# Kernel optimization log

Hardware: AMD Instinct MI355X
Metric: run time of the kernel (lower is better)

Reference implementation:

```python
import jax, jax.numpy as jnp
import numpy as np
import math

DEPTH = 3
RATIO = 0.5
EPS = 1e-5


def _mlp_ln(h, W1, b1, W2, b2, W3, b3, g, beta):
    h = jax.nn.gelu(h @ W1 + b1, approximate=False)
    h = jax.nn.gelu(h @ W2 + b2, approximate=False)
    h = h @ W3 + b3
    mu = jnp.mean(h, axis=-1, keepdims=True)
    var = jnp.mean((h - mu) ** 2, axis=-1, keepdims=True)
    return g * (h - mu) * jax.lax.rsqrt(var + EPS) + beta


def _node_to_node(x, s, r, n, p):
    # two-way gather -> scatter_add -> MLP+LN. Row n of x_pad is a zero dummy
    # node that absorbs edges dropped by pooling (fixed-size, jit-friendly).
    x_pad = jnp.concatenate([x, jnp.zeros((1, x.shape[1]), x.dtype)], axis=0)
    msg = x_pad[jnp.concatenate([s, r])]            # [2E, C]
    recv = jnp.concatenate([r, s])                  # [2E]
    agg = jax.ops.segment_sum(msg, recv, num_segments=n + 1)[:n]
    return _mlp_ln(agg, *p)


def _forward(x, senders, receivers, pool_w, down_p, up_p):
    s, r = senders, receivers
    xs, edges, perms = [x], [(s, r)], []
    n = x.shape[0]
    for i in range(DEPTH):
        k = math.ceil(RATIO * n)  # PyG topk: ceil(ratio * N)
        w = pool_w[i]
        score = jnp.tanh(x @ w / jnp.linalg.norm(w))
        vals, perm = jax.lax.top_k(score, k)
        x = x[perm] * vals[:, None]
        # remap edges; dropped nodes (and old dummy n) map to new dummy k
        nmap = jnp.full((n + 1,), k, dtype=s.dtype).at[perm].set(
            jnp.arange(k, dtype=s.dtype))
        ns_, nr_ = nmap[s], nmap[r]
        invalid = (ns_ == k) | (nr_ == k)
        s = jnp.where(invalid, k, ns_)
        r = jnp.where(invalid, k, nr_)
        x = _node_to_node(x, s, r, k, down_p[i])
        if i < DEPTH - 1:
            xs.append(x)
            edges.append((s, r))
        perms.append(perm)
        n = k
    for i in range(DEPTH):
        j = DEPTH - 1 - i
        res = xs[j]
        s, r = edges[j]
        perm = perms[j]
        up = jnp.zeros_like(res).at[perm].set(x)
        x = jnp.concatenate([res, up], axis=-1)  # sum_res=False -> concat
        x = _node_to_node(x, s, r, res.shape[0], up_p[i])
    return x


def setup_inputs() -> dict:
    key = jax.random.key(0)
    ks = jax.random.split(key, 16)
    N, E, C, D = 50000, 600000, 128, DEPTH
    f32 = jnp.float32

    def lin(k, fi, fo):
        return (jax.random.normal(k, (D, fi, fo), f32) / np.sqrt(fi)).astype(f32)

    return {
        'x': jax.random.normal(ks[0], (N, C), f32),
        'senders': jax.random.randint(ks[1], (E,), 0, N, dtype=jnp.int32),
        'receivers': jax.random.randint(ks[2], (E,), 0, N, dtype=jnp.int32),
        'pool_w': jax.random.normal(ks[3], (D, C), f32),
        'down_W1': lin(ks[4], C, C), 'down_b1': jnp.zeros((D, C), f32),
        'down_W2': lin(ks[5], C, C), 'down_b2': jnp.zeros((D, C), f32),
        'down_W3': lin(ks[6], C, C), 'down_b3': jnp.zeros((D, C), f32),
        'down_g': jnp.ones((D, C), f32), 'down_beta': jnp.zeros((D, C), f32),
        'up_W1': lin(ks[7], 2 * C, C), 'up_b1': jnp.zeros((D, C), f32),
        'up_W2': lin(ks[8], C, C), 'up_b2': jnp.zeros((D, C), f32),
        'up_W3': lin(ks[9], C, C), 'up_b3': jnp.zeros((D, C), f32),
        'up_g': jnp.ones((D, C), f32), 'up_beta': jnp.zeros((D, C), f32),
    }


def reference(x, senders, receivers, pool_w,
              down_W1, down_b1, down_W2, down_b2, down_W3, down_b3,
              down_g, down_beta,
              up_W1, up_b1, up_W2, up_b2, up_W3, up_b3, up_g, up_beta):
    down_p = [(down_W1[i], down_b1[i], down_W2[i], down_b2[i],
               down_W3[i], down_b3[i], down_g[i], down_beta[i])
              for i in range(DEPTH)]
    up_p = [(up_W1[i], up_b1[i], up_W2[i], up_b2[i],
             up_W3[i], up_b3[i], up_g[i], up_beta[i])
            for i in range(DEPTH)]
    return _forward(x, senders, receivers, pool_w, down_p, up_p)
```

## Files before the change

### kernel.cpp

```cpp
#include <hip/hip_runtime.h>
#include <math.h>


typedef unsigned short u16;
typedef short bf16x8 __attribute__((ext_vector_type(8)));
typedef float f32x4 __attribute__((ext_vector_type(4)));

#define HIST_STRIDE (2 * 65536 + 512)
#define NB 128
#define NB_LOG 7
#define SUBR 5000

__device__ __forceinline__ unsigned int fkey(float f) {
  unsigned int b = __float_as_uint(f);
  return (b & 0x80000000u) ? ~b : (b | 0x80000000u);
}

__device__ __forceinline__ float gelu_f(float v) {
  return 0.5f * v * (1.0f + erff(v * 0.70710678118654752f));
}

__device__ __forceinline__ u16 f2bf(float f) {
  unsigned u = __float_as_uint(f);
  u = (u + 0x7FFFu + ((u >> 16) & 1u)) >> 16;
  return (u16)u;
}
__device__ __forceinline__ float bf2f(u16 u) {
  return __uint_as_float(((unsigned)u) << 16);
}

__global__ void score_kernel(const float* __restrict__ x, const float* __restrict__ w,
                             float* __restrict__ key, float* __restrict__ valt, int n) {
  int wave = threadIdx.x >> 6, lane = threadIdx.x & 63;
  int i = blockIdx.x * 4 + wave;
  if (i >= n) return;
  float2 xv = *(const float2*)&x[(size_t)i * 128 + lane * 2];
  float2 wv = *(const float2*)&w[lane * 2];
  double d  = (double)xv.x * wv.x + (double)xv.y * wv.y;
  double nw = (double)wv.x * wv.x + (double)wv.y * wv.y;
  for (int o = 32; o; o >>= 1) { d += __shfl_down(d, o, 64); nw += __shfl_down(nw, o, 64); }
  if (lane == 0) {
    key[i]  = (float)d;
    valt[i] = (float)tanh(d / sqrt(nw));
  }
}

__global__ void preamble_kernel(const float* __restrict__ x, u16* __restrict__ xb, int n,
                                const float* __restrict__ uW1, const float* __restrict__ uW2,
                                const float* __restrict__ uW3, u16* __restrict__ wt1,
                                u16* __restrict__ wt2, u16* __restrict__ wt3,
                                const float* __restrict__ poolw, double* __restrict__ sqn,
                                u16* __restrict__ z0, u16* __restrict__ z1,
                                u16* __restrict__ z2, int* __restrict__ histAll,
                                int nbX, int nbHZ, int nHist) {
  int b = blockIdx.x;
  if (b < nbX) {
    int gid = b * 256 + threadIdx.x;
    if (gid < n * 32) {
      float4 a = *(const float4*)&x[(size_t)gid * 4];
      *(ushort4*)&xb[(size_t)gid * 4] =
          make_ushort4(f2bf(a.x), f2bf(a.y), f2bf(a.z), f2bf(a.w));
    }
    return;
  }
  b -= nbX;
  if (b < 768) {
    int i = b * 256 + threadIdx.x;
    int lvl = i >> 16, rem = i & 65535;
    if (rem < 32768) {
      int k = rem >> 7, c = rem & 127;
      wt1[(size_t)lvl * 32768 + c * 256 + k] = f2bf(uW1[(size_t)lvl * 32768 + rem]);
    } else if (rem < 49152) {
      int j = rem - 32768; int k = j >> 7, c = j & 127;
      wt2[(size_t)lvl * 16384 + c * 128 + k] = f2bf(uW2[(size_t)lvl * 16384 + j]);
    } else {
      int j = rem - 49152; int k = j >> 7, c = j & 127;
      wt3[(size_t)lvl * 16384 + c * 128 + k] = f2bf(uW3[(size_t)lvl * 16384 + j]);
    }
    return;
  }
  b -= 768;
  if (b == 0) {
    if (threadIdx.x < 64) {
      int lane = threadIdx.x;
      for (int l = 0; l < 3; ++l) {
        float2 wv = *(const float2*)&poolw[l * 128 + lane * 2];
        double nw = (double)wv.x * wv.x + (double)wv.y * wv.y;
        for (int o = 32; o; o >>= 1) nw += __shfl_down(nw, o, 64);
        if (lane == 0) sqn[l] = sqrt(nw);
      }
    }
    return;
  }
  b -= 1;
  if (b == 0) {
    int t = threadIdx.x;
    if (t < 128) { z0[t] = 0; z1[t] = 0; z2[t] = 0; }
    return;
  }
  b -= 1;
  {
    int i = b * 256 + threadIdx.x;
    if (i < nHist) histAll[i] = 0;
  }
}

__global__ void hist_hi_kernel(const float* __restrict__ key, int* __restrict__ hist,
                               int* __restrict__ csum, int n) {
  __shared__ int lc[256];
  lc[threadIdx.x] = 0;
  __syncthreads();
  int i = blockIdx.x * 256 + threadIdx.x;
  if (i < n) {
    unsigned b = fkey(key[i]) >> 16;
    atomicAdd(&hist[b], 1);
    atomicAdd(&lc[b >> 8], 1);
  }
  __syncthreads();
  int v = lc[threadIdx.x];
  if (v) atomicAdd(&csum[threadIdx.x], v);
}

__global__ void hist_lo_kernel(const float* __restrict__ key, const int* __restrict__ meta,
                               int* __restrict__ hist, int* __restrict__ csum, int n) {
  __shared__ int lc[256];
  lc[threadIdx.x] = 0;
  __syncthreads();
  int i = blockIdx.x * 256 + threadIdx.x;
  if (i < n) {
    unsigned u = fkey(key[i]);
    if ((u >> 16) == (unsigned)meta[0]) {
      unsigned b = u & 0xFFFFu;
      atomicAdd(&hist[b], 1);
      atomicAdd(&lc[b >> 8], 1);
    }
  }
  __syncthreads();
  int v = lc[threadIdx.x];
  if (v) atomicAdd(&csum[threadIdx.x], v);
}

__device__ __forceinline__ void suffix_scan256(int* sA, int t) {
  for (int o = 1; o < 256; o <<= 1) {
    int add = (t + o < 256) ? sA[t + o] : 0;
    __syncthreads();
    sA[t] += add;
    __syncthreads();
  }
}

__global__ void find_hi2_kernel(const int* __restrict__ hist, const int* __restrict__ csum,
                                int* __restrict__ meta, int k) {
  __shared__ int sA[256];
  __shared__ int cSh, cumSh;
  int t = threadIdx.x;
  sA[t] = csum[t];
  __syncthreads();
  suffix_scan256(sA, t);
  int nxt = (t == 255) ? 0 : sA[t + 1];
  if (sA[t] >= k && nxt < k) { cSh = t; cumSh = nxt; }
  __syncthreads();
  int c = cSh;
  int k2 = k - cumSh;
  sA[t] = hist[c * 256 + t];
  __syncthreads();
  suffix_scan256(sA, t);
  nxt = (t == 255) ? 0 : sA[t + 1];
  if (sA[t] >= k2 && nxt < k2) {
    meta[0] = c * 256 + t;
    meta[1] = k2 - nxt;
  }
}

__global__ void find_lo2_kernel(const int* __restrict__ hist, const int* __restrict__ csum,
                                int* __restrict__ meta) {
  __shared__ int sA[256];
  __shared__ int cSh, cumSh;
  int t = threadIdx.x;
  int m = meta[1], B = meta[0];
  sA[t] = csum[t];
  __syncthreads();
  suffix_scan256(sA, t);
  int nxt = (t == 255) ? 0 : sA[t + 1];
  if (sA[t] >= m && nxt < m) { cSh = t; cumSh = nxt; }
  __syncthreads();
  int c = cSh;
  int m2 = m - cumSh;
  sA[t] = hist[c * 256 + t];
  __syncthreads();
  suffix_scan256(sA, t);
  nxt = (t == 255) ? 0 : sA[t + 1];
  if (sA[t] >= m2 && nxt < m2) {
    meta[3] = (int)((((unsigned)B) << 16) | (unsigned)(c * 256 + t));
    meta[4] = m2 - nxt;
  }
  if (t == 0) meta[5] = 0;
}

__global__ void tie_count_kernel(const float* __restrict__ key, const int* __restrict__ meta,
                                 int* __restrict__ tcnt, int n) {
  __shared__ int cnt[4];
  unsigned uT = (unsigned)meta[3];
  int i = blockIdx.x * 256 + threadIdx.x;
  bool tie = (i < n) && (fkey(key[i]) == uT);
  unsigned long long m = __ballot(tie);
  int lane = threadIdx.x & 63, w = threadIdx.x >> 6;
  if (lane == 0) cnt[w] = __popcll(m);
  __syncthreads();
  if (threadIdx.x == 0) tcnt[blockIdx.x] = cnt[0] + cnt[1] + cnt[2] + cnt[3];
}

__global__ void tie_select_kernel(const float* __restrict__ key, const float* __restrict__ valt,
                                  const int* __restrict__ tcnt, int* __restrict__ meta,
                                  int* __restrict__ perm, float* __restrict__ vals,
                                  int* __restrict__ nmap, int n, int k) {
  __shared__ int red[256];
  __shared__ int woff[4];
  int t = threadIdx.x;
  red[t] = (t < (int)blockIdx.x) ? tcnt[t] : 0;
  __syncthreads();
  for (int s = 128; s; s >>= 1) {
    if (t < s) red[t] += red[t + s];
    __syncthreads();
  }
  int blockbase = red[0];
  unsigned uT = (unsigned)meta[3];
  int tsel = meta[4];
  int i = blockIdx.x * 256 + t;
  unsigned u = (i < n) ? fkey(key[i]) : 0u;
  bool tie = (i < n) && (u == uT);
  unsigned long long m = __ballot(tie);
  int lane = t & 63, w = t >> 6;
  if (lane == 0) woff[w] = __popcll(m);
  __syncthreads();
  if (t == 0) {
    int c = 0;
    for (int q = 0; q < 4; ++q) { int v = woff[q]; woff[q] = c; c += v; }
  }
  __syncthreads();
  if (i > n) return;
  if (i == n) { nmap[n] = k; return; }
  bool sel;
  if (tie) {
    int pre = __popcll(m & ((1ull << lane) - 1ull));
    int rank = blockbase + woff[w] + pre;
    sel = (rank < tsel);
  } else {
    sel = (u > uT);
  }
  if (sel) {
    int slot = atomicAdd(&meta[5], 1);
    perm[slot] = i; vals[slot] = valt[i]; nmap[i] = slot;
  } else {
    nmap[i] = k;
  }
}

__global__ void pool_kernel(const float* __restrict__ x, const int* __restrict__ perm,
                            const float* __restrict__ vals, float* __restrict__ xp, int k) {
  int gid = blockIdx.x * 256 + threadIdx.x;
  int t = gid >> 5;
  if (t >= k) return;
  int c = (gid & 31) << 2;
  float v = vals[t];
  float4 a = *(const float4*)&x[(size_t)perm[t] * 128 + c];
  a.x *= v; a.y *= v; a.z *= v; a.w *= v;
  *(float4*)&xp[(size_t)t * 128 + c] = a;
}

__global__ void csr_count_kernel(const int* __restrict__ s, const int* __restrict__ r,
                                 int* __restrict__ H, int N, int E, int CH) {
  __shared__ int cnt[SUBR];
  int b = blockIdx.x & (NB - 1);
  int sub = blockIdx.x >> NB_LOG;
  int base = sub * SUBR;
  int top = base + SUBR; if (top > N) top = N;
  int span = top - base;
  for (int t = threadIdx.x; t < span; t += 256) cnt[t] = 0;
  __syncthreads();
  int lo = b * CH, hi = lo + CH; if (hi > E) hi = E;
  for (int e = lo + threadIdx.x; e < hi; e += 256) {
    int sv = s[e], rv = r[e];
    if ((unsigned)(rv - base) < (unsigned)span) atomicAdd(&cnt[rv - base], 1);
    if ((unsigned)(sv - base) < (unsigned)span) atomicAdd(&cnt[sv - base], 1);
  }
  __syncthreads();
  int* Hb = H + (size_t)b * N + base;
  for (int t = threadIdx.x; t < span; t += 256) Hb[t] = cnt[t];
}

__global__ void colsum_part_kernel(const int* __restrict__ H, int* __restrict__ deg,
                                   int* __restrict__ bsum, int n) {
  __shared__ int l[256];
  int i = blockIdx.x * 256 + threadIdx.x;
  int v = 0;
  if (i < n) {
#pragma unroll 4
    for (int b = 0; b < NB; ++b) v += H[(size_t)b * n + i];
    deg[i] = v;
  }
  l[threadIdx.x] = (i < n) ? v : 0;
  __syncthreads();
  for (int s = 128; s; s >>= 1) {
    if (threadIdx.x < s) l[threadIdx.x] += l[threadIdx.x + s];
    __syncthreads();
  }
  if (threadIdx.x == 0) bsum[blockIdx.x] = l[0];
}

__global__ void scanfix_kernel(const int* __restrict__ deg, const int* __restrict__ bsum,
                               int* __restrict__ off, int* __restrict__ H, int n) {
  __shared__ int red[256];
  __shared__ int l[256];
  int i = blockIdx.x * 256 + threadIdx.x;
  int t = threadIdx.x;
  red[t] = (t < (int)blockIdx.x) ? bsum[t] : 0;
  __syncthreads();
  for (int s = 128; s; s >>= 1) {
    if (t < s) red[t] += red[t + s];
    __syncthreads();
  }
  int base = red[0];
  int v = (i < n) ? deg[i] : 0;
  l[t] = v;
  __syncthreads();
#pragma unroll
  for (int s = 1; s < 256; s <<= 1) {
    int add = (t >= s) ? l[t - s] : 0;
    __syncthreads();
    l[t] += add;
    __syncthreads();
  }
  int incl = l[t];
  if (i < n) {
    int e = base + incl - v;
    off[i] = e;
    if (i == n - 1) off[n] = base + incl;
    int run = e;
#pragma unroll 4
    for (int b = 0; b < NB; ++b) {
      size_t id = (size_t)b * n + i;
      int tv = H[id];
      H[id] = run;
      run += tv;
    }
  }
}

__global__ void csr_scatter_lds_kernel(const int* __restrict__ s, const int* __restrict__ r,
                                       const int* __restrict__ H, int* __restrict__ idx,
                                       int N, int E, int CH) {
  __shared__ int cnt[SUBR];
  int b = blockIdx.x & (NB - 1);
  int sub = blockIdx.x >> NB_LOG;
  int base = sub * SUBR;
  int top = base + SUBR; if (top > N) top = N;
  int span = top - base;
  for (int t = threadIdx.x; t < span; t += 256) cnt[t] = 0;
  __syncthreads();
  int lo = b * CH, hi = lo + CH; if (hi > E) hi = E;
  const int* Hb = H + (size_t)b * N;
  for (int e = lo + threadIdx.x; e < hi; e += 256) {
    int sv = s[e], rv = r[e];
    if ((unsigned)(rv - base) < (unsigned)span) {
      int loc = atomicAdd(&cnt[rv - base], 1);
      idx[Hb[rv] + loc] = sv;
    }
    if ((unsigned)(sv - base) < (unsigned)span) {
      int loc = atomicAdd(&cnt[sv - base], 1);
      idx[Hb[sv] + loc] = rv;
    }
  }
}

__global__ void derive_deg_kernel(const int* __restrict__ permL, const int* __restrict__ nm,
                                  const int* __restrict__ offP, const int* __restrict__ idxP,
                                  int* __restrict__ deg, int k) {
  int wave = threadIdx.x >> 6, lane = threadIdx.x & 63;
  int v = blockIdx.x * 4 + wave;
  if (v >= k) return;
  int p = permL[v];
  int lo = __builtin_amdgcn_readfirstlane(offP[p]);
  int hi = __builtin_amdgcn_readfirstlane(offP[p + 1]);
  int cnt = 0;
  for (int j0 = lo; j0 < hi; j0 += 64) {
    int j = j0 + lane;
    bool ok = (j < hi) && (nm[idxP[j]] < k);
    unsigned long long msk = __ballot(ok);
    cnt += __popcll(msk);
  }
  if (lane == 0) deg[v] = cnt;
}

__global__ void derive_fill_kernel(const int* __restrict__ permL, const int* __restrict__ nm,
                                   const int* __restrict__ offP, const int* __restrict__ idxP,
                                   const int* __restrict__ offL, int* __restrict__ idxL,
                                   int k) {
  int wave = threadIdx.x >> 6, lane = threadIdx.x & 63;
  int v = blockIdx.x * 4 + wave;
  if (v >= k) return;
  int p = permL[v];
  int lo = __builtin_amdgcn_readfirstlane(offP[p]);
  int hi = __builtin_amdgcn_readfirstlane(offP[p + 1]);
  int base = __builtin_amdgcn_readfirstlane(offL[v]);
  for (int j0 = lo; j0 < hi; j0 += 64) {
    int j = j0 + lane;
    int m = k;
    if (j < hi) m = nm[idxP[j]];
    bool ok = m < k;
    unsigned long long msk = __ballot(ok);
    int rank = __popcll(msk & ((1ull << lane) - 1ull));
    if (ok) idxL[base + rank] = m;
    base += __popcll(msk);
  }
}

__global__ void scan_part_kernel(const int* __restrict__ deg, int* __restrict__ bsum, int n) {
  __shared__ int l[256];
  int i = blockIdx.x * 256 + threadIdx.x;
  l[threadIdx.x] = (i < n) ? deg[i] : 0;
  __syncthreads();
  for (int s = 128; s; s >>= 1) {
    if (threadIdx.x < s) l[threadIdx.x] += l[threadIdx.x + s];
    __syncthreads();
  }
  if (threadIdx.x == 0) bsum[blockIdx.x] = l[0];
}

__global__ void scan_final_kernel(const int* __restrict__ deg, const int* __restrict__ bsum,
                                  int* __restrict__ off, int n) {
  __shared__ int red[256];
  __shared__ int l[256];
  int i = blockIdx.x * 256 + threadIdx.x;
  int t = threadIdx.x;
  red[t] = (t < (int)blockIdx.x) ? bsum[t] : 0;
  __syncthreads();
  for (int s = 128; s; s >>= 1) {
    if (t < s) red[t] += red[t + s];
    __syncthreads();
  }
  int base = red[0];
  int v = (i < n) ? deg[i] : 0;
  l[t] = v;
  __syncthreads();
#pragma unroll
  for (int s = 1; s < 256; s <<= 1) {
    int add = (t >= s) ? l[t - s] : 0;
    __syncthreads();
    l[t] += add;
    __syncthreads();
  }
  int incl = l[t];
  if (i < n) {
    int e = base + incl - v;
    off[i] = e;
    if (i == n - 1) off[n] = base + incl;
  }
}

__global__ void idxup3_kernel(const int* __restrict__ idxA, const int* __restrict__ nmA,
                              const int* __restrict__ lenA, int* __restrict__ outA,
                              const int* __restrict__ idxB, const int* __restrict__ nmB,
                              const int* __restrict__ lenB, int* __restrict__ outB,
                              const int* __restrict__ idxC, const int* __restrict__ nmC,
                              const int* __restrict__ lenC, int* __restrict__ outC,
                              int nbSeg, int maxlen) {
  int seg = blockIdx.x / nbSeg;
  int j = (blockIdx.x - seg * nbSeg) * 256 + threadIdx.x;
  if (j >= maxlen) return;
  const int* idx; const int* nm; const int* len; int* out;
  if (seg == 0)      { idx = idxA; nm = nmA; len = lenA; out = outA; }
  else if (seg == 1) { idx = idxB; nm = nmB; len = lenB; out = outB; }
  else               { idx = idxC; nm = nmC; len = lenC; out = outC; }
  if (j >= len[0]) return;
  out[j] = nm[idx[j]];
}

__global__ void agg_kernel(const float* __restrict__ x, const int* __restrict__ off,
                           const int* __restrict__ idx, float* __restrict__ agg, int n) {
  int wave = threadIdx.x >> 6, lane = threadIdx.x & 63;
  int v = blockIdx.x * 4 + wave;
  if (v >= n) return;
  int lo = __builtin_amdgcn_readfirstlane(off[v]);
  int hi = __builtin_amdgcn_readfirstlane(off[v + 1]);
  int g = lane >> 5, sl = lane & 31;
  const float* bp = x + sl * 4;
  float4 acc = {0.f, 0.f, 0.f, 0.f};
#define ACC_F(EE)                                        \
  do {                                                   \
    float4 w_ = *(const float4*)(bp + (size_t)(EE) * 128);\
    acc.x += w_.x; acc.y += w_.y; acc.z += w_.z; acc.w += w_.w; \
  } while (0)
  int j = lo;
  for (; j + 8 <= hi; j += 8) {
    int q0 = idx[j],     q1 = idx[j + 1], q2 = idx[j + 2], q3 = idx[j + 3];
    int q4 = idx[j + 4], q5 = idx[j + 5], q6 = idx[j + 6], q7 = idx[j + 7];
    ACC_F(g ? q1 : q0);
    ACC_F(g ? q3 : q2);
    ACC_F(g ? q5 : q4);
    ACC_F(g ? q7 : q6);
  }
  for (; j + 2 <= hi; j += 2) {
    int q0 = idx[j], q1 = idx[j + 1];
    ACC_F(g ? q1 : q0);
  }
  if (j < hi) {
    int q0 = idx[j];
    if (!g) ACC_F(q0);
  }
#undef ACC_F
  acc.x += __shfl_xor(acc.x, 32, 64);
  acc.y += __shfl_xor(acc.y, 32, 64);
  acc.z += __shfl_xor(acc.z, 32, 64);
  acc.w += __shfl_xor(acc.w, 32, 64);
  if (!g) *(float4*)&agg[(size_t)v * 128 + sl * 4] = acc;
}

template <int OFS>
__global__ void agg_gather_kernel(const u16* __restrict__ tab, const int* __restrict__ idx,
                                  const int* __restrict__ off, u16* __restrict__ agg, int n) {
  int wave = threadIdx.x >> 6, lane = threadIdx.x & 63;
  int v = blockIdx.x * 4 + wave;
  if (v >= n) return;
  int lo = __builtin_amdgcn_readfirstlane(off[v]);
  int hi = __builtin_amdgcn_readfirstlane(off[v + 1]);
  int g = lane >> 4, sl = lane & 15;
  const u16* bp = tab + sl * 8;
  float4 a0 = {0.f, 0.f, 0.f, 0.f}, a1 = {0.f, 0.f, 0.f, 0.f};

#define ACC_ROW(EE)                                     \
  do {                                                  \
    uint4 wq = *(const uint4*)(bp + (size_t)(EE) * 128);\
    a0.x += __uint_as_float(wq.x << 16);                \
    a0.y += __uint_as_float(wq.x & 0xffff0000u);        \
    a0.z += __uint_as_float(wq.y << 16);                \
    a0.w += __uint_as_float(wq.y & 0xffff0000u);        \
    a1.x += __uint_as_float(wq.z << 16);                \
    a1.y += __uint_as_float(wq.z & 0xffff0000u);        \
    a1.z += __uint_as_float(wq.w << 16);                \
    a1.w += __uint_as_float(wq.w & 0xffff0000u);        \
  } while (0)

  int j = lo;
  for (; j + 16 <= hi; j += 16) {
    int e0 = idx[j + g];
    int e1 = idx[j + g + 4];
    int e2 = idx[j + g + 8];
    int e3 = idx[j + g + 12];
    ACC_ROW(e0); ACC_ROW(e1); ACC_ROW(e2); ACC_ROW(e3);
  }
  for (; j + 4 <= hi; j += 4) {
    int e0 = idx[j + g];
    ACC_ROW(e0);
  }
  int rmn = hi - j;
  if (g < rmn) {
    int e = idx[j + g];
    ACC_ROW(e);
  }
#undef ACC_ROW

  a0.x += __shfl_xor(a0.x, 16, 64);
  a0.y += __shfl_xor(a0.y, 16, 64);
  a0.z += __shfl_xor(a0.z, 16, 64);
  a0.w += __shfl_xor(a0.w, 16, 64);
  a1.x += __shfl_xor(a1.x, 16, 64);
  a1.y += __shfl_xor(a1.y, 16, 64);
  a1.z += __shfl_xor(a1.z, 16, 64);
  a1.w += __shfl_xor(a1.w, 16, 64);
  a0.x += __shfl_xor(a0.x, 32, 64);
  a0.y += __shfl_xor(a0.y, 32, 64);
  a0.z += __shfl_xor(a0.z, 32, 64);
  a0.w += __shfl_xor(a0.w, 32, 64);
  a1.x += __shfl_xor(a1.x, 32, 64);
  a1.y += __shfl_xor(a1.y, 32, 64);
  a1.z += __shfl_xor(a1.z, 32, 64);
  a1.w += __shfl_xor(a1.w, 32, 64);

  if (lane < 16) {
    bf16x8 ov;
    ov[0] = (short)f2bf(a0.x); ov[1] = (short)f2bf(a0.y);
    ov[2] = (short)f2bf(a0.z); ov[3] = (short)f2bf(a0.w);
    ov[4] = (short)f2bf(a1.x); ov[5] = (short)f2bf(a1.y);
    ov[6] = (short)f2bf(a1.z); ov[7] = (short)f2bf(a1.w);
    *(bf16x8*)&agg[(size_t)v * 256 + OFS + sl * 8] = ov;
  }
}

template <bool GELU>
__global__ __launch_bounds__(256) void gemm_kernel(const float* __restrict__ A,
                                                   const float* __restrict__ W,
                                                   const float* __restrict__ bias,
                                                   float* __restrict__ out, int n) {
  __shared__ float As[32 * 32];
  __shared__ float Ws[32 * 128];
  int t = threadIdx.x;
  int row0 = blockIdx.x * 32;
  int colg = (t & 31) << 2;
  int rowg = (t >> 5) << 2;
  float acc[4][4];
#pragma unroll
  for (int i = 0; i < 4; ++i)
#pragma unroll
    for (int j = 0; j < 4; ++j) acc[i][j] = 0.f;

  for (int k0 = 0; k0 < 128; k0 += 32) {
    __syncthreads();
    {
      int ar = t >> 3, ac = (t & 7) << 2;
      float4 av = make_float4(0.f, 0.f, 0.f, 0.f);
      if (row0 + ar < n) av = *(const float4*)&A[(size_t)(row0 + ar) * 128 + k0 + ac];
      *(float4*)&As[ar * 32 + ac] = av;
    }
#pragma unroll
    for (int l = 0; l < 4; ++l) {
      int id = t + l * 256;
      int kk = id >> 5, wc = (id & 31) << 2;
      *(float4*)&Ws[kk * 128 + wc] = *(const float4*)&W[(size_t)(k0 + kk) * 128 + wc];
    }
    __syncthreads();
#pragma unroll
    for (int kk = 0; kk < 32; kk += 4) {
      float4 wv[4];
#pragma unroll
      for (int j = 0; j < 4; ++j) wv[j] = *(const float4*)&Ws[(kk + j) * 128 + colg];
#pragma unroll
      for (int i = 0; i < 4; ++i) {
        float4 av = *(const float4*)&As[(rowg + i) * 32 + kk];
        acc[i][0] += av.x * wv[0].x + av.y * wv[1].x + av.z * wv[2].x + av.w * wv[3].x;
        acc[i][1] += av.x * wv[0].y + av.y * wv[1].y + av.z * wv[2].y + av.w * wv[3].y;
        acc[i][2] += av.x * wv[0].z + av.y * wv[1].z + av.z * wv[2].z + av.w * wv[3].z;
        acc[i][3] += av.x * wv[0].w + av.y * wv[1].w + av.z * wv[2].w + av.w * wv[3].w;
      }
    }
  }
  float4 bv = *(const float4*)&bias[colg];
#pragma unroll
  for (int i = 0; i < 4; ++i) {
    int rr = row0 + rowg + i;
    if (rr < n) {
      float4 o = make_float4(acc[i][0] + bv.x, acc[i][1] + bv.y, acc[i][2] + bv.z, acc[i][3] + bv.w);
      if (GELU) { o.x = gelu_f(o.x); o.y = gelu_f(o.y); o.z = gelu_f(o.z); o.w = gelu_f(o.w); }
      *(float4*)&out[(size_t)rr * 128 + colg] = o;
    }
  }
}

template <int K>
__global__ __launch_bounds__(256) void gemm_mfma_kernel(const u16* __restrict__ A,
                                                        const u16* __restrict__ WT,
                                                        const float* __restrict__ bias,
                                                        u16* __restrict__ out, int n) {
  __shared__ u16 As[64 * 72];
  __shared__ u16 Ws[128 * 72];
  int t = threadIdx.x;
  int lane = t & 63, wave = t >> 6;
  int row0 = blockIdx.x * 64;
  f32x4 acc[8];
#pragma unroll
  for (int i = 0; i < 8; ++i) acc[i] = (f32x4){0.f, 0.f, 0.f, 0.f};

  for (int k0 = 0; k0 < K; k0 += 64) {
    __syncthreads();
#pragma unroll
    for (int i = 0; i < 2; ++i) {
      int c = t + i * 256;
      int r = c >> 3, seg = c & 7;
      bf16x8 v = {0, 0, 0, 0, 0, 0, 0, 0};
      if (row0 + r < n) v = *(const bf16x8*)&A[(size_t)(row0 + r) * K + k0 + seg * 8];
      *(bf16x8*)&As[r * 72 + seg * 8] = v;
    }
#pragma unroll
    for (int i = 0; i < 4; ++i) {
      int c = t + i * 256;
      int r = c >> 3, seg = c & 7;
      *(bf16x8*)&Ws[r * 72 + seg * 8] = *(const bf16x8*)&WT[(size_t)r * K + k0 + seg * 8];
    }
    __syncthreads();
#pragma unroll
    for (int kk = 0; kk < 64; kk += 32) {
      bf16x8 a = *(const bf16x8*)&As[(wave * 16 + (lane & 15)) * 72 + kk + (lane >> 4) * 8];
#pragma unroll
      for (int ct = 0; ct < 8; ++ct) {
        bf16x8 b = *(const bf16x8*)&Ws[(ct * 16 + (lane & 15)) * 72 + kk + (lane >> 4) * 8];
        acc[ct] = __builtin_amdgcn_mfma_f32_16x16x32_bf16(a, b, acc[ct], 0, 0, 0);
      }
    }
  }
  int colb = lane & 15, rquad = lane >> 4;
#pragma unroll
  for (int ct = 0; ct < 8; ++ct) {
#pragma unroll
    for (int r = 0; r < 4; ++r) {
      int row = row0 + wave * 16 + rquad * 4 + r;
      if (row < n) {
        int col = ct * 16 + colb;
        out[(size_t)row * 128 + col] = f2bf(gelu_f(acc[ct][r] + bias[col]));
      }
    }
  }
}

template <bool WF32, bool WBF>
__global__ __launch_bounds__(256) void gemm_mfma_ln_kernel(
    const u16* __restrict__ A, const u16* __restrict__ WT, const float* __restrict__ bias,
    const float* __restrict__ g, const float* __restrict__ beta,
    float* __restrict__ out, u16* __restrict__ outbf, int n) {
  __shared__ u16 As[64 * 72];
  __shared__ u16 Ws[128 * 72];
  int t = threadIdx.x;
  int lane = t & 63, wave = t >> 6;
  int row0 = blockIdx.x * 64;
  f32x4 acc[8];
#pragma unroll
  for (int i = 0; i < 8; ++i) acc[i] = (f32x4){0.f, 0.f, 0.f, 0.f};

  for (int k0 = 0; k0 < 128; k0 += 64) {
    __syncthreads();
#pragma unroll
    for (int i = 0; i < 2; ++i) {
      int c = t + i * 256;
      int r = c >> 3, seg = c & 7;
      bf16x8 v = {0, 0, 0, 0, 0, 0, 0, 0};
      if (row0 + r < n) v = *(const bf16x8*)&A[(size_t)(row0 + r) * 128 + k0 + seg * 8];
      *(bf16x8*)&As[r * 72 + seg * 8] = v;
    }
#pragma unroll
    for (int i = 0; i < 4; ++i) {
      int c = t + i * 256;
      int r = c >> 3, seg = c & 7;
      *(bf16x8*)&Ws[r * 72 + seg * 8] = *(const bf16x8*)&WT[(size_t)r * 128 + k0 + seg * 8];
    }
    __syncthreads();
#pragma unroll
    for (int kk = 0; kk < 64; kk += 32) {
      bf16x8 a = *(const bf16x8*)&As[(wave * 16 + (lane & 15)) * 72 + kk + (lane >> 4) * 8];
#pragma unroll
      for (int ct = 0; ct < 8; ++ct) {
        bf16x8 b = *(const bf16x8*)&Ws[(ct * 16 + (lane & 15)) * 72 + kk + (lane >> 4) * 8];
        acc[ct] = __builtin_amdgcn_mfma_f32_16x16x32_bf16(a, b, acc[ct], 0, 0, 0);
      }
    }
  }
  int colb = lane & 15, rquad = lane >> 4;
  float bv[8], gv[8], bev[8];
#pragma unroll
  for (int ct = 0; ct < 8; ++ct) {
    int col = ct * 16 + colb;
    bv[ct] = bias[col]; gv[ct] = g[col]; bev[ct] = beta[col];
  }
#pragma unroll
  for (int r = 0; r < 4; ++r) {
    float s1 = 0.f;
#pragma unroll
    for (int ct = 0; ct < 8; ++ct) s1 += acc[ct][r] + bv[ct];
#pragma unroll
    for (int o = 1; o <= 8; o <<= 1) s1 += __shfl_xor(s1, o, 64);
    float mu = s1 * (1.0f / 128.0f);
    float s2 = 0.f;
#pragma unroll
    for (int ct = 0; ct < 8; ++ct) { float d = acc[ct][r] + bv[ct] - mu; s2 += d * d; }
#pragma unroll
    for (int o = 1; o <= 8; o <<= 1) s2 += __shfl_xor(s2, o, 64);
    float rs = rsqrtf(s2 * (1.0f / 128.0f) + 1e-5f);
    int row = row0 + wave * 16 + rquad * 4 + r;
    if (row < n) {
#pragma unroll
      for (int ct = 0; ct < 8; ++ct) {
        int col = ct * 16 + colb;
        float o = gv[ct] * (acc[ct][r] + bv[ct] - mu) * rs + bev[ct];
        if (WF32) out[(size_t)row * 128 + col] = o;
        if (WBF)  outbf[(size_t)row * 128 + col] = f2bf(o);
      }
    }
  }
}

template <bool SCORE, bool WBF>
__global__ void ln_kernel(const float* __restrict__ h, const float* __restrict__ g,
                          const float* __restrict__ beta, float* __restrict__ out,
                          u16* __restrict__ outbf, const float* __restrict__ wnext,
                          const double* __restrict__ sqn, float* __restrict__ key,
                          float* __restrict__ valt, int n) {
  int wave = threadIdx.x >> 6, lane = threadIdx.x & 63;
  int i = blockIdx.x * 4 + wave;
  if (i >= n) return;
  float2 hv = *(const float2*)&h[(size_t)i * 128 + lane * 2];
  float s = hv.x + hv.y;
  for (int o = 32; o; o >>= 1) s += __shfl_down(s, o, 64);
  float mu = __shfl(s, 0, 64) * (1.0f / 128.0f);
  float dx = hv.x - mu, dy = hv.y - mu;
  float q = dx * dx + dy * dy;
  for (int o = 32; o; o >>= 1) q += __shfl_down(q, o, 64);
  float var = __shfl(q, 0, 64) * (1.0f / 128.0f);
  float rs = rsqrtf(var + 1e-5f);
  float2 gv = *(const float2*)&g[lane * 2];
  float2 bv = *(const float2*)&beta[lane * 2];
  float2 o2; o2.x = gv.x * dx * rs + bv.x; o2.y = gv.y * dy * rs + bv.y;
  *(float2*)&out[(size_t)i * 128 + lane * 2] = o2;
  if (WBF)
    *(ushort2*)&outbf[(size_t)i * 128 + lane * 2] = make_ushort2(f2bf(o2.x), f2bf(o2.y));
  if (SCORE) {
    float2 wv = *(const float2*)&wnext[lane * 2];
    double d = (double)o2.x * wv.x + (double)o2.y * wv.y;
    for (int o = 32; o; o >>= 1) d += __shfl_down(d, o, 64);
    if (lane == 0) {
      key[i]  = (float)d;
      valt[i] = (float)tanh(d / sqn[0]);
    }
  }
}


static inline int cdiv(int a, int b) { return (a + b - 1) / b; }

extern "C" void kernel_launch(void* const* d_in, const int* in_sizes, int n_in,
                              void* d_out, int out_size, void* d_ws, size_t ws_size,
                              hipStream_t stream) {
  const float* x0   = (const float*)d_in[0];
  const int*   snd  = (const int*)d_in[1];
  const int*   rcv  = (const int*)d_in[2];
  const float* poolw = (const float*)d_in[3];
  const float* dW1 = (const float*)d_in[4];
  const float* db1 = (const float*)d_in[5];
  const float* dW2 = (const float*)d_in[6];
  const float* db2 = (const float*)d_in[7];
  const float* dW3 = (const float*)d_in[8];
  const float* db3 = (const float*)d_in[9];
  const float* dg  = (const float*)d_in[10];
  const float* dbe = (const float*)d_in[11];
  const float* uW1 = (const float*)d_in[12];
  const float* ub1 = (const float*)d_in[13];
  const float* uW2 = (const float*)d_in[14];
  const float* ub2 = (const float*)d_in[15];
  const float* uW3 = (const float*)d_in[16];
  const float* ub3 = (const float*)d_in[17];
  const float* ug  = (const float*)d_in[18];
  const float* ube = (const float*)d_in[19];

  const int N0 = in_sizes[0] / 128;
  const int E  = in_sizes[1];
  const int N1 = (N0 + 1) / 2, N2 = (N1 + 1) / 2, N3 = (N2 + 1) / 2;

  char* p = (char*)d_ws;
  auto alloc = [&](size_t bytes) -> void* {
    void* r = (void*)p;
    p += (bytes + 255) & ~(size_t)255;
    return r;
  };
  float* key  = (float*)alloc((size_t)N0 * 4);
  float* valt = (float*)alloc((size_t)N0 * 4);
  int*   histAll = (int*)alloc((size_t)3 * HIST_STRIDE * 4);
  int*   meta = (int*)alloc(64 * 4);
  int*   tcnt = (int*)alloc(512 * 4);
  int*   bsum = (int*)alloc(256 * 4);
  int*   nm1 = (int*)alloc((size_t)(N0 + 1) * 4);
  int*   nm2 = (int*)alloc((size_t)(N1 + 1) * 4);
  int*   nm3 = (int*)alloc((size_t)(N2 + 1) * 4);
  int*   perm0 = (int*)alloc((size_t)N1 * 4);
  int*   perm1 = (int*)alloc((size_t)N2 * 4);
  int*   perm2 = (int*)alloc((size_t)N3 * 4);
  float* vals  = (float*)alloc((size_t)N1 * 4);
  double* sqn  = (double*)alloc(8 * 8);
  float* x1 = (float*)alloc((size_t)N1 * 128 * 4);
  float* x2 = (float*)alloc((size_t)N2 * 128 * 4);
  float* x3 = (float*)alloc((size_t)N3 * 128 * 4);
  float* xp = (float*)alloc((size_t)N1 * 128 * 4);
  float* aggf = (float*)alloc((size_t)N1 * 128 * 4);
  float* h1f  = (float*)alloc((size_t)N1 * 128 * 4);
  float* h2f  = (float*)alloc((size_t)N1 * 128 * 4);
  u16* agg_bf = (u16*)alloc((size_t)N0 * 256 * 2);
  u16* res0_bf = (u16*)alloc((size_t)N0 * 128 * 2);
  u16* res1_bf = (u16*)alloc((size_t)N1 * 128 * 2);
  u16* res2_bf = (u16*)alloc((size_t)N2 * 128 * 2);
  u16* x3_bf   = (u16*)alloc((size_t)(N3 + 1) * 128 * 2);
  u16* xu2_bf  = (u16*)alloc((size_t)(N2 + 1) * 128 * 2);
  u16* xu1_bf  = (u16*)alloc((size_t)(N1 + 1) * 128 * 2);
  u16* wt1 = (u16*)alloc((size_t)3 * 128 * 256 * 2);
  u16* wt2 = (u16*)alloc((size_t)3 * 128 * 128 * 2);
  u16* wt3 = (u16*)alloc((size_t)3 * 128 * 128 * 2);
  int* degAll = (int*)alloc((size_t)(N0 + N1 + N2 + N3) * 4);
  int* deg0 = degAll;
  int* deg1 = degAll + N0;
  int* deg2 = deg1 + N1;
  int* deg3 = deg2 + N2;
  int* off0 = (int*)alloc((size_t)(N0 + 1) * 4);
  int* idx0 = (int*)alloc((size_t)2 * E * 4);
  int* off1 = (int*)alloc((size_t)(N1 + 1) * 4);
  int* idx1 = (int*)alloc((size_t)2 * E * 4);
  int* off2 = (int*)alloc((size_t)(N2 + 1) * 4);
  int* idx2 = (int*)alloc((size_t)2 * E * 4);
  int* off3 = (int*)alloc((size_t)(N3 + 1) * 4);
  int* idx3 = (int*)alloc((size_t)2 * E * 4);
  int* idxu0 = (int*)alloc((size_t)2 * E * 4);
  int* idxu1 = (int*)alloc((size_t)2 * E * 4);
  int* idxu2 = (int*)alloc((size_t)2 * E * 4);
  int* H = (int*)alloc((size_t)NB * N0 * 4);
  u16* h1b = (u16*)xp;
  u16* h2b = (u16*)alloc((size_t)N0 * 128 * 2);

  auto run_scan = [&](int* degB, int* offB, int n) {
    int nb = cdiv(n, 256);
    scan_part_kernel<<<nb, 256, 0, stream>>>(degB, bsum, n);
    scan_final_kernel<<<nb, 256, 0, stream>>>(degB, bsum, offB, n);
  };

  {
    int nbX = cdiv(N0 * 32, 256);
    int nHist = 3 * HIST_STRIDE;
    int nbHZ = cdiv(nHist, 256);
    preamble_kernel<<<nbX + 768 + 1 + 1 + nbHZ, 256, 0, stream>>>(
        x0, res0_bf, N0, uW1, uW2, uW3, wt1, wt2, wt3, poolw, sqn,
        x3_bf + (size_t)N3 * 128, xu2_bf + (size_t)N2 * 128,
        xu1_bf + (size_t)N1 * 128, histAll, nbX, nbHZ, nHist);
  }

  {
    int nSub = cdiv(N0, SUBR);
    int CH = cdiv(E, NB);
    int nbN = cdiv(N0, 256);
    csr_count_kernel<<<NB * nSub, 256, 0, stream>>>(snd, rcv, H, N0, E, CH);
    colsum_part_kernel<<<nbN, 256, 0, stream>>>(H, deg0, bsum, N0);
    scanfix_kernel<<<nbN, 256, 0, stream>>>(deg0, bsum, off0, H, N0);
    csr_scatter_lds_kernel<<<NB * nSub, 256, 0, stream>>>(snd, rcv, H, idx0, N0, E, CH);
  }

  auto down_step = [&](int n, int k, const float* xcur, int* permL, int* nmL,
                       float* xnext, u16* xnext_bf, int lvl,
                       const int* offP, const int* idxP,
                       int* offL, int* degL, int* idxL) {
    int nb = cdiv(n, 256);
    int* histL = histAll + (size_t)lvl * HIST_STRIDE;
    int* csum_hi = histL + 2 * 65536;
    int* csum_lo = csum_hi + 256;
    hist_hi_kernel<<<nb, 256, 0, stream>>>(key, histL, csum_hi, n);
    find_hi2_kernel<<<1, 256, 0, stream>>>(histL, csum_hi, meta, k);
    hist_lo_kernel<<<nb, 256, 0, stream>>>(key, meta, histL + 65536, csum_lo, n);
    find_lo2_kernel<<<1, 256, 0, stream>>>(histL + 65536, csum_lo, meta);
    tie_count_kernel<<<nb, 256, 0, stream>>>(key, meta, tcnt, n);
    tie_select_kernel<<<cdiv(n + 1, 256), 256, 0, stream>>>(
        key, valt, tcnt, meta, permL, vals, nmL, n, k);
    pool_kernel<<<cdiv(k * 32, 256), 256, 0, stream>>>(xcur, permL, vals, xp, k);
    derive_deg_kernel<<<cdiv(k, 4), 256, 0, stream>>>(permL, nmL, offP, idxP, degL, k);
    run_scan(degL, offL, k);
    derive_fill_kernel<<<cdiv(k, 4), 256, 0, stream>>>(permL, nmL, offP, idxP, offL, idxL, k);
    agg_kernel<<<cdiv(k, 4), 256, 0, stream>>>(xp, offL, idxL, aggf, k);
    gemm_kernel<true><<<cdiv(k, 32), 256, 0, stream>>>(
        aggf, dW1 + (size_t)lvl * 128 * 128, db1 + (size_t)lvl * 128, h1f, k);
    gemm_kernel<true><<<cdiv(k, 32), 256, 0, stream>>>(
        h1f, dW2 + (size_t)lvl * 128 * 128, db2 + (size_t)lvl * 128, h2f, k);
    gemm_kernel<false><<<cdiv(k, 32), 256, 0, stream>>>(
        h2f, dW3 + (size_t)lvl * 128 * 128, db3 + (size_t)lvl * 128, h1f, k);
    if (lvl < 2)
      ln_kernel<true, true><<<cdiv(k, 4), 256, 0, stream>>>(
          h1f, dg + (size_t)lvl * 128, dbe + (size_t)lvl * 128, xnext, xnext_bf,
          poolw + (size_t)(lvl + 1) * 128, sqn + (lvl + 1), key, valt, k);
    else
      ln_kernel<false, true><<<cdiv(k, 4), 256, 0, stream>>>(
          h1f, dg + (size_t)lvl * 128, dbe + (size_t)lvl * 128, xnext, xnext_bf,
          nullptr, nullptr, nullptr, nullptr, k);
  };

  score_kernel<<<cdiv(N0, 4), 256, 0, stream>>>(x0, poolw, key, valt, N0);
  down_step(N0, N1, x0, perm0, nm1, x1, res1_bf, 0, off0, idx0, off1, deg1, idx1);
  down_step(N1, N2, x1, perm1, nm2, x2, res2_bf, 1, off1, idx1, off2, deg2, idx2);
  down_step(N2, N3, x2, perm2, nm3, x3, x3_bf,   2, off2, idx2, off3, deg3, idx3);

  {
    int nbSeg = cdiv(2 * E, 256);
    idxup3_kernel<<<3 * nbSeg, 256, 0, stream>>>(
        idx2, nm3, off2 + N2, idxu2,
        idx1, nm2, off1 + N1, idxu1,
        idx0, nm1, off0 + N0, idxu0, nbSeg, 2 * E);
  }

  auto up_step = [&](int n, const u16* resb, const u16* xdb, int lvl,
                     const int* offL, const int* idxL, const int* idxUL,
                     bool wantF32, float* outF32, u16* outBF) {
    agg_gather_kernel<0><<<cdiv(n, 4), 256, 0, stream>>>(resb, idxL, offL, agg_bf, n);
    agg_gather_kernel<128><<<cdiv(n, 4), 256, 0, stream>>>(xdb, idxUL, offL, agg_bf, n);
    gemm_mfma_kernel<256><<<cdiv(n, 64), 256, 0, stream>>>(
        agg_bf, wt1 + (size_t)lvl * 128 * 256, ub1 + (size_t)lvl * 128, h1b, n);
    gemm_mfma_kernel<128><<<cdiv(n, 64), 256, 0, stream>>>(
        h1b, wt2 + (size_t)lvl * 128 * 128, ub2 + (size_t)lvl * 128, h2b, n);
    if (wantF32)
      gemm_mfma_ln_kernel<true, false><<<cdiv(n, 64), 256, 0, stream>>>(
          h2b, wt3 + (size_t)lvl * 128 * 128, ub3 + (size_t)lvl * 128,
          ug + (size_t)lvl * 128, ube + (size_t)lvl * 128, outF32, nullptr, n);
    else
      gemm_mfma_ln_kernel<false, true><<<cdiv(n, 64), 256, 0, stream>>>(
          h2b, wt3 + (size_t)lvl * 128 * 128, ub3 + (size_t)lvl * 128,
          ug + (size_t)lvl * 128, ube + (size_t)lvl * 128, nullptr, outBF, n);
  };

  up_step(N2, res2_bf, x3_bf,  0, off2, idx2, idxu2, false, nullptr, xu2_bf);
  up_step(N1, res1_bf, xu2_bf, 1, off1, idx1, idxu1, false, nullptr, xu1_bf);
  up_step(N0, res0_bf, xu1_bf, 2, off0, idx0, idxu0, true, (float*)d_out, nullptr);

  (void)n_in; (void)out_size; (void)ws_size;
}
```

Before: 831.2 us.

## Fuse up-path three-layer MLP+LN into one kernel and merge gathers

Replaces the three separate GEMM launches of each up-step (two GELU GEMMs and one GEMM+LayerNorm) with a single kernel. Hidden activations stay in shared memory as bf16, so the h1/h2 round trips through global memory go away. The two half-gather launches (residual and upsampled) are also merged into one launch that picks its table by block index. In exchange the fused kernel uses more LDS (about 35KB), which may lower occupancy, and it serialises the weight loads of the three layers.

```diff
diff --git a/kernel.cpp b/kernel.cpp
--- a/kernel.cpp
+++ b/kernel.cpp
@@ -516,11 +516,17 @@
   if (!g) *(float4*)&agg[(size_t)v * 128 + sl * 4] = acc;
 }
 
-template <int OFS>
-__global__ void agg_gather_kernel(const u16* __restrict__ tab, const int* __restrict__ idx,
-                                  const int* __restrict__ off, u16* __restrict__ agg, int n) {
+__global__ void agg_gather2_kernel(const u16* __restrict__ tabR, const int* __restrict__ idxR,
+                                   const u16* __restrict__ tabU, const int* __restrict__ idxU,
+                                   const int* __restrict__ off, u16* __restrict__ agg,
+                                   int n, int nbHalf) {
+  bool upH = (int)blockIdx.x >= nbHalf;
+  int blk = upH ? (int)blockIdx.x - nbHalf : (int)blockIdx.x;
+  const u16* tab = upH ? tabU : tabR;
+  const int* idx = upH ? idxU : idxR;
+  int OFS = upH ? 128 : 0;
   int wave = threadIdx.x >> 6, lane = threadIdx.x & 63;
-  int v = blockIdx.x * 4 + wave;
+  int v = blk * 4 + wave;
   if (v >= n) return;
   int lo = __builtin_amdgcn_readfirstlane(off[v]);
   int hi = __builtin_amdgcn_readfirstlane(off[v + 1]);
@@ -642,136 +648,6 @@
       float4 o = make_float4(acc[i][0] + bv.x, acc[i][1] + bv.y, acc[i][2] + bv.z, acc[i][3] + bv.w);
       if (GELU) { o.x = gelu_f(o.x); o.y = gelu_f(o.y); o.z = gelu_f(o.z); o.w = gelu_f(o.w); }
       *(float4*)&out[(size_t)rr * 128 + colg] = o;
-    }
-  }
-}
-
-template <int K>
-__global__ __launch_bounds__(256) void gemm_mfma_kernel(const u16* __restrict__ A,
-                                                        const u16* __restrict__ WT,
-                                                        const float* __restrict__ bias,
-                                                        u16* __restrict__ out, int n) {
-  __shared__ u16 As[64 * 72];
-  __shared__ u16 Ws[128 * 72];
-  int t = threadIdx.x;
-  int lane = t & 63, wave = t >> 6;
-  int row0 = blockIdx.x * 64;
-  f32x4 acc[8];
-#pragma unroll
-  for (int i = 0; i < 8; ++i) acc[i] = (f32x4){0.f, 0.f, 0.f, 0.f};
-
-  for (int k0 = 0; k0 < K; k0 += 64) {
-    __syncthreads();
-#pragma unroll
-    for (int i = 0; i < 2; ++i) {
-      int c = t + i * 256;
-      int r = c >> 3, seg = c & 7;
-      bf16x8 v = {0, 0, 0, 0, 0, 0, 0, 0};
-      if (row0 + r < n) v = *(const bf16x8*)&A[(size_t)(row0 + r) * K + k0 + seg * 8];
-      *(bf16x8*)&As[r * 72 + seg * 8] = v;
-    }
-#pragma unroll
-    for (int i = 0; i < 4; ++i) {
-      int c = t + i * 256;
-      int r = c >> 3, seg = c & 7;
-      *(bf16x8*)&Ws[r * 72 + seg * 8] = *(const bf16x8*)&WT[(size_t)r * K + k0 + seg * 8];
-    }
-    __syncthreads();
-#pragma unroll
-    for (int kk = 0; kk < 64; kk += 32) {
-      bf16x8 a = *(const bf16x8*)&As[(wave * 16 + (lane & 15)) * 72 + kk + (lane >> 4) * 8];
-#pragma unroll
-      for (int ct = 0; ct < 8; ++ct) {
-        bf16x8 b = *(const bf16x8*)&Ws[(ct * 16 + (lane & 15)) * 72 + kk + (lane >> 4) * 8];
-        acc[ct] = __builtin_amdgcn_mfma_f32_16x16x32_bf16(a, b, acc[ct], 0, 0, 0);
-      }
-    }
-  }
-  int colb = lane & 15, rquad = lane >> 4;
-#pragma unroll
-  for (int ct = 0; ct < 8; ++ct) {
-#pragma unroll
-    for (int r = 0; r < 4; ++r) {
-      int row = row0 + wave * 16 + rquad * 4 + r;
-      if (row < n) {
-        int col = ct * 16 + colb;
-        out[(size_t)row * 128 + col] = f2bf(gelu_f(acc[ct][r] + bias[col]));
-      }
-    }
-  }
-}
-
-template <bool WF32, bool WBF>
-__global__ __launch_bounds__(256) void gemm_mfma_ln_kernel(
-    const u16* __restrict__ A, const u16* __restrict__ WT, const float* __restrict__ bias,
-    const float* __restrict__ g, const float* __restrict__ beta,
-    float* __restrict__ out, u16* __restrict__ outbf, int n) {
-  __shared__ u16 As[64 * 72];
-  __shared__ u16 Ws[128 * 72];
-  int t = threadIdx.x;
-  int lane = t & 63, wave = t >> 6;
-  int row0 = blockIdx.x * 64;
-  f32x4 acc[8];
-#pragma unroll
-  for (int i = 0; i < 8; ++i) acc[i] = (f32x4){0.f, 0.f, 0.f, 0.f};
-
-  for (int k0 = 0; k0 < 128; k0 += 64) {
-    __syncthreads();
-#pragma unroll
-    for (int i = 0; i < 2; ++i) {
-      int c = t + i * 256;
-      int r = c >> 3, seg = c & 7;
-      bf16x8 v = {0, 0, 0, 0, 0, 0, 0, 0};
-      if (row0 + r < n) v = *(const bf16x8*)&A[(size_t)(row0 + r) * 128 + k0 + seg * 8];
-      *(bf16x8*)&As[r * 72 + seg * 8] = v;
-    }
-#pragma unroll
-    for (int i = 0; i < 4; ++i) {
-      int c = t + i * 256;
-      int r = c >> 3, seg = c & 7;
-      *(bf16x8*)&Ws[r * 72 + seg * 8] = *(const bf16x8*)&WT[(size_t)r * 128 + k0 + seg * 8];
-    }
-    __syncthreads();
-#pragma unroll
-    for (int kk = 0; kk < 64; kk += 32) {
-      bf16x8 a = *(const bf16x8*)&As[(wave * 16 + (lane & 15)) * 72 + kk + (lane >> 4) * 8];
-#pragma unroll
-      for (int ct = 0; ct < 8; ++ct) {
-        bf16x8 b = *(const bf16x8*)&Ws[(ct * 16 + (lane & 15)) * 72 + kk + (lane >> 4) * 8];
-        acc[ct] = __builtin_amdgcn_mfma_f32_16x16x32_bf16(a, b, acc[ct], 0, 0, 0);
-      }
-    }
-  }
-  int colb = lane & 15, rquad = lane >> 4;
-  float bv[8], gv[8], bev[8];
-#pragma unroll
-  for (int ct = 0; ct < 8; ++ct) {
-    int col = ct * 16 + colb;
-    bv[ct] = bias[col]; gv[ct] = g[col]; bev[ct] = beta[col];
-  }
-#pragma unroll
-  for (int r = 0; r < 4; ++r) {
-    float s1 = 0.f;
-#pragma unroll
-    for (int ct = 0; ct < 8; ++ct) s1 += acc[ct][r] + bv[ct];
-#pragma unroll
-    for (int o = 1; o <= 8; o <<= 1) s1 += __shfl_xor(s1, o, 64);
-    float mu = s1 * (1.0f / 128.0f);
-    float s2 = 0.f;
-#pragma unroll
-    for (int ct = 0; ct < 8; ++ct) { float d = acc[ct][r] + bv[ct] - mu; s2 += d * d; }
-#pragma unroll
-    for (int o = 1; o <= 8; o <<= 1) s2 += __shfl_xor(s2, o, 64);
-    float rs = rsqrtf(s2 * (1.0f / 128.0f) + 1e-5f);
-    int row = row0 + wave * 16 + rquad * 4 + r;
-    if (row < n) {
-#pragma unroll
-      for (int ct = 0; ct < 8; ++ct) {
-        int col = ct * 16 + colb;
-        float o = gv[ct] * (acc[ct][r] + bv[ct] - mu) * rs + bev[ct];
-        if (WF32) out[(size_t)row * 128 + col] = o;
-        if (WBF)  outbf[(size_t)row * 128 + col] = f2bf(o);
-      }
     }
   }
 }
@@ -807,6 +683,151 @@
     if (lane == 0) {
       key[i]  = (float)d;
       valt[i] = (float)tanh(d / sqn[0]);
+    }
+  }
+}
+
+template <bool WF32, bool WBF>
+__global__ __launch_bounds__(256) void mlp_up_kernel(
+    const u16* __restrict__ A,
+    const u16* __restrict__ WT1, const float* __restrict__ b1,
+    const u16* __restrict__ WT2, const float* __restrict__ b2,
+    const u16* __restrict__ WT3, const float* __restrict__ b3,
+    const float* __restrict__ g, const float* __restrict__ beta,
+    float* __restrict__ out, u16* __restrict__ outbf, int n) {
+  __shared__ u16 As[64 * 72];
+  __shared__ u16 Ws[128 * 72];
+  __shared__ u16 cur[64 * 136];
+  int t = threadIdx.x;
+  int lane = t & 63, wave = t >> 6;
+  int row0 = blockIdx.x * 64;
+  int colb = lane & 15, rquad = lane >> 4;
+  f32x4 acc[8];
+
+#pragma unroll
+  for (int i = 0; i < 8; ++i) acc[i] = (f32x4){0.f, 0.f, 0.f, 0.f};
+  for (int k0 = 0; k0 < 256; k0 += 64) {
+    __syncthreads();
+#pragma unroll
+    for (int i = 0; i < 2; ++i) {
+      int c = t + i * 256;
+      int r = c >> 3, seg = c & 7;
+      bf16x8 v = {0, 0, 0, 0, 0, 0, 0, 0};
+      if (row0 + r < n) v = *(const bf16x8*)&A[(size_t)(row0 + r) * 256 + k0 + seg * 8];
+      *(bf16x8*)&As[r * 72 + seg * 8] = v;
+    }
+#pragma unroll
+    for (int i = 0; i < 4; ++i) {
+      int c = t + i * 256;
+      int r = c >> 3, seg = c & 7;
+      *(bf16x8*)&Ws[r * 72 + seg * 8] = *(const bf16x8*)&WT1[(size_t)r * 256 + k0 + seg * 8];
+    }
+    __syncthreads();
+#pragma unroll
+    for (int kk = 0; kk < 64; kk += 32) {
+      bf16x8 a = *(const bf16x8*)&As[(wave * 16 + (lane & 15)) * 72 + kk + (lane >> 4) * 8];
+#pragma unroll
+      for (int ct = 0; ct < 8; ++ct) {
+        bf16x8 b = *(const bf16x8*)&Ws[(ct * 16 + (lane & 15)) * 72 + kk + (lane >> 4) * 8];
+        acc[ct] = __builtin_amdgcn_mfma_f32_16x16x32_bf16(a, b, acc[ct], 0, 0, 0);
+      }
+    }
+  }
+  __syncthreads();
+#pragma unroll
+  for (int ct = 0; ct < 8; ++ct) {
+    int col = ct * 16 + colb;
+    float bb = b1[col];
+#pragma unroll
+    for (int r = 0; r < 4; ++r) {
+      int row = wave * 16 + rquad * 4 + r;
+      cur[row * 136 + col] = f2bf(gelu_f(acc[ct][r] + bb));
+    }
+  }
+
+#pragma unroll
+  for (int i = 0; i < 8; ++i) acc[i] = (f32x4){0.f, 0.f, 0.f, 0.f};
+  for (int k0 = 0; k0 < 128; k0 += 64) {
+    __syncthreads();
+#pragma unroll
+    for (int i = 0; i < 4; ++i) {
+      int c = t + i * 256;
+      int r = c >> 3, seg = c & 7;
+      *(bf16x8*)&Ws[r * 72 + seg * 8] = *(const bf16x8*)&WT2[(size_t)r * 128 + k0 + seg * 8];
+    }
+    __syncthreads();
+#pragma unroll
+    for (int kk = 0; kk < 64; kk += 32) {
+      bf16x8 a = *(const bf16x8*)&cur[(wave * 16 + (lane & 15)) * 136 + k0 + kk + (lane >> 4) * 8];
+#pragma unroll
+      for (int ct = 0; ct < 8; ++ct) {
+        bf16x8 b = *(const bf16x8*)&Ws[(ct * 16 + (lane & 15)) * 72 + kk + (lane >> 4) * 8];
+        acc[ct] = __builtin_amdgcn_mfma_f32_16x16x32_bf16(a, b, acc[ct], 0, 0, 0);
+      }
+    }
+  }
+  __syncthreads();
+#pragma unroll
+  for (int ct = 0; ct < 8; ++ct) {
+    int col = ct * 16 + colb;
+    float bb = b2[col];
+#pragma unroll
+    for (int r = 0; r < 4; ++r) {
+      int row = wave * 16 + rquad * 4 + r;
+      cur[row * 136 + col] = f2bf(gelu_f(acc[ct][r] + bb));
+    }
+  }
+
+#pragma unroll
+  for (int i = 0; i < 8; ++i) acc[i] = (f32x4){0.f, 0.f, 0.f, 0.f};
+  for (int k0 = 0; k0 < 128; k0 += 64) {
+    __syncthreads();
+#pragma unroll
+    for (int i = 0; i < 4; ++i) {
+      int c = t + i * 256;
+      int r = c >> 3, seg = c & 7;
+      *(bf16x8*)&Ws[r * 72 + seg * 8] = *(const bf16x8*)&WT3[(size_t)r * 128 + k0 + seg * 8];
+    }
+    __syncthreads();
+#pragma unroll
+    for (int kk = 0; kk < 64; kk += 32) {
+      bf16x8 a = *(const bf16x8*)&cur[(wave * 16 + (lane & 15)) * 136 + k0 + kk + (lane >> 4) * 8];
+#pragma unroll
+      for (int ct = 0; ct < 8; ++ct) {
+        bf16x8 b = *(const bf16x8*)&Ws[(ct * 16 + (lane & 15)) * 72 + kk + (lane >> 4) * 8];
+        acc[ct] = __builtin_amdgcn_mfma_f32_16x16x32_bf16(a, b, acc[ct], 0, 0, 0);
+      }
+    }
+  }
+  float bv[8], gv[8], bev[8];
+#pragma unroll
+  for (int ct = 0; ct < 8; ++ct) {
+    int col = ct * 16 + colb;
+    bv[ct] = b3[col]; gv[ct] = g[col]; bev[ct] = beta[col];
+  }
+#pragma unroll
+  for (int r = 0; r < 4; ++r) {
+    float s1 = 0.f;
+#pragma unroll
+    for (int ct = 0; ct < 8; ++ct) s1 += acc[ct][r] + bv[ct];
+#pragma unroll
+    for (int o = 1; o <= 8; o <<= 1) s1 += __shfl_xor(s1, o, 64);
+    float mu = s1 * (1.0f / 128.0f);
+    float s2 = 0.f;
+#pragma unroll
+    for (int ct = 0; ct < 8; ++ct) { float d = acc[ct][r] + bv[ct] - mu; s2 += d * d; }
+#pragma unroll
+    for (int o = 1; o <= 8; o <<= 1) s2 += __shfl_xor(s2, o, 64);
+    float rs = rsqrtf(s2 * (1.0f / 128.0f) + 1e-5f);
+    int row = row0 + wave * 16 + rquad * 4 + r;
+    if (row < n) {
+#pragma unroll
+      for (int ct = 0; ct < 8; ++ct) {
+        int col = ct * 16 + colb;
+        float o = gv[ct] * (acc[ct][r] + bv[ct] - mu) * rs + bev[ct];
+        if (WF32) out[(size_t)row * 128 + col] = o;
+        if (WBF)  outbf[(size_t)row * 128 + col] = f2bf(o);
+      }
     }
   }
 }
@@ -896,14 +917,6 @@
   int* idxu1 = (int*)alloc((size_t)2 * E * 4);
   int* idxu2 = (int*)alloc((size_t)2 * E * 4);
   int* H = (int*)alloc((size_t)NB * N0 * 4);
-  u16* h1b = (u16*)xp;
-  u16* h2b = (u16*)alloc((size_t)N0 * 128 * 2);
-
-  auto run_scan = [&](int* degB, int* offB, int n) {
-    int nb = cdiv(n, 256);
-    scan_part_kernel<<<nb, 256, 0, stream>>>(degB, bsum, n);
-    scan_final_kernel<<<nb, 256, 0, stream>>>(degB, bsum, offB, n);
-  };
 
   {
     int nbX = cdiv(N0 * 32, 256);
@@ -924,6 +937,12 @@
     scanfix_kernel<<<nbN, 256, 0, stream>>>(deg0, bsum, off0, H, N0);
     csr_scatter_lds_kernel<<<NB * nSub, 256, 0, stream>>>(snd, rcv, H, idx0, N0, E, CH);
   }
+
+  auto run_scan = [&](int* degB, int* offB, int n) {
+    int nb = cdiv(n, 256);
+    scan_part_kernel<<<nb, 256, 0, stream>>>(degB, bsum, n);
+    scan_final_kernel<<<nb, 256, 0, stream>>>(degB, bsum, offB, n);
+  };
 
   auto down_step = [&](int n, int k, const float* xcur, int* permL, int* nmL,
                        float* xnext, u16* xnext_bf, int lvl,
@@ -977,20 +996,25 @@
   auto up_step = [&](int n, const u16* resb, const u16* xdb, int lvl,
                      const int* offL, const int* idxL, const int* idxUL,
                      bool wantF32, float* outF32, u16* outBF) {
-    agg_gather_kernel<0><<<cdiv(n, 4), 256, 0, stream>>>(resb, idxL, offL, agg_bf, n);
-    agg_gather_kernel<128><<<cdiv(n, 4), 256, 0, stream>>>(xdb, idxUL, offL, agg_bf, n);
-    gemm_mfma_kernel<256><<<cdiv(n, 64), 256, 0, stream>>>(
-        agg_bf, wt1 + (size_t)lvl * 128 * 256, ub1 + (size_t)lvl * 128, h1b, n);
-    gemm_mfma_kernel<128><<<cdiv(n, 64), 256, 0, stream>>>(
-        h1b, wt2 + (size_t)lvl * 128 * 128, ub2 + (size_t)lvl * 128, h2b, n);
+    int nbh = cdiv(n, 4);
+    agg_gather2_kernel<<<2 * nbh, 256, 0, stream>>>(
+        resb, idxL, xdb, idxUL, offL, agg_bf, n, nbh);
     if (wantF32)
-      gemm_mfma_ln_kernel<true, false><<<cdiv(n, 64), 256, 0, stream>>>(
-          h2b, wt3 + (size_t)lvl * 128 * 128, ub3 + (size_t)lvl * 128,
-          ug + (size_t)lvl * 128, ube + (size_t)lvl * 128, outF32, nullptr, n);
+      mlp_up_kernel<true, false><<<cdiv(n, 64), 256, 0, stream>>>(
+          agg_bf,
+          wt1 + (size_t)lvl * 128 * 256, ub1 + (size_t)lvl * 128,
+          wt2 + (size_t)lvl * 128 * 128, ub2 + (size_t)lvl * 128,
+          wt3 + (size_t)lvl * 128 * 128, ub3 + (size_t)lvl * 128,
+          ug + (size_t)lvl * 128, ube + (size_t)lvl * 128,
+          outF32, nullptr, n);
     else
-      gemm_mfma_ln_kernel<false, true><<<cdiv(n, 64), 256, 0, stream>>>(
-          h2b, wt3 + (size_t)lvl * 128 * 128, ub3 + (size_t)lvl * 128,
-          ug + (size_t)lvl * 128, ube + (size_t)lvl * 128, nullptr, outBF, n);
+      mlp_up_kernel<false, true><<<cdiv(n, 64), 256, 0, stream>>>(
+          agg_bf,
+          wt1 + (size_t)lvl * 128 * 256, ub1 + (size_t)lvl * 128,
+          wt2 + (size_t)lvl * 128 * 128, ub2 + (size_t)lvl * 128,
+          wt3 + (size_t)lvl * 128 * 128, ub3 + (size_t)lvl * 128,
+          ug + (size_t)lvl * 128, ube + (size_t)lvl * 128,
+          nullptr, outBF, n);
   };
 
   up_step(N2, res2_bf, x3_bf,  0, off2, idx2, idxu2, false, nullptr, xu2_bf);
```

New measurement: 779.7 us. 6.2% less time.
